# Performance work log

Hardware: AMD Instinct MI355X
Metric: run time of the kernel (lower is better)

The kernel has to match this reference:

```python
import jax, jax.numpy as jnp
import numpy as np

N, TP, E = 8, 2048, 4096
S = 8            # 2**spatial_dim
C = 64           # sqrt(embed_dim)
T = TP * S       # 16384
V = 16           # num_vocab


def setup_inputs() -> dict:
    key = jax.random.key(0)
    ks = jax.random.split(key, 9)
    x = jax.random.normal(ks[0], (N, TP, E), dtype=jnp.float32)
    value = jax.random.randint(ks[1], (N, T), 0, 4, dtype=jnp.int64)
    depth = jnp.sort(jax.random.randint(ks[2], (N, T), 0, 16, dtype=jnp.int64), axis=1)
    pos = jax.random.randint(ks[3], (N, T, 3), 0, 32, dtype=jnp.int64)
    # ConvTranspose1d(E, C, kernel=S, stride=S): weight [E, C, S]
    W1 = jax.random.normal(ks[4], (E, C, S), dtype=jnp.float32) / np.sqrt(E)
    b1 = jax.random.normal(ks[5], (C,), dtype=jnp.float32) * 0.01
    # ConvTranspose1d(C, 1, kernel=S, stride=S): weight [C, 1, S]
    W2 = jax.random.normal(ks[6], (C, 1, S), dtype=jnp.float32) / np.sqrt(C)
    b2 = jax.random.normal(ks[7], (1,), dtype=jnp.float32) * 0.01
    # Linear(1, V+1, bias=False): weight [V+1, 1]
    W3 = jax.random.normal(ks[8], (V + 1, 1), dtype=jnp.float32)
    return {"x": x, "value": value, "depth": depth, "pos": pos,
            "W1": W1, "b1": b1, "W2": W2, "b2": b2, "W3": W3}


def reference(x, value, depth, pos, W1, b1, W2, b2, W3):
    n, tp, e = x.shape
    s = W1.shape[2]
    t = value.shape[1]  # = tp * s
    posn = jnp.arange(t)
    # Truncate each value sequence at argmax(depth); pad_sequence pads with 0.
    idx = jnp.argmax(depth, axis=1)                      # [N]
    val_pad = jnp.where(posn[None, :] < idx[:, None], value, 0)  # [N, T]
    # deconv_1: stride == kernel -> non-overlapping expansion
    x1 = jnp.einsum('nte,ecs->ntsc', x, W1).reshape(n, t, -1) + b1  # [N, T, C]
    # Per-sample masked gather (val==2), compacted to front, zero-padded
    mask = val_pad == 2                                   # [N, T]
    order = jnp.argsort(jnp.logical_not(mask), axis=1, stable=True)  # True first
    y = jnp.take_along_axis(x1, order[:, :, None], axis=1)           # [N, T, C]
    counts = mask.sum(axis=1)                             # [N]
    y = jnp.where((posn[None, :] < counts[:, None])[:, :, None], y, 0.0)
    # deconv_2: [N, T, C] -> [N, T*S, 1]
    y2 = jnp.einsum('ntc,cs->nts', y, W2[:, 0, :]).reshape(n, t * s, 1) + b2
    # linear (no bias): [N, T*S, V+1]
    return y2 @ W3.T
```

## Files before the change

### kernel.cpp

```cpp
#include <hip/hip_runtime.h>

#define N_    8
#define TP_   2048
#define E_    4096
#define S_    8
#define C_    64
#define T_    16384
#define TS_   131072
#define OUTW  17
#define OUT_ELEMS 17825792
#define F4_PER_N 557056
#define F4_TOTAL 4456448

typedef __attribute__((ext_vector_type(8))) short short8;
typedef __attribute__((ext_vector_type(4))) float float4v;

static __device__ __forceinline__ unsigned short f2bf(float f) {
    unsigned int u = __builtin_bit_cast(unsigned int, f);
    u += 0x7FFFu + ((u >> 16) & 1u);
    return (unsigned short)(u >> 16);
}

__global__ __launch_bounds__(256) void prep_kernel(
    const float* __restrict__ W1, const float* __restrict__ b1,
    const float* __restrict__ W2, const float* __restrict__ b2,
    unsigned short* __restrict__ Bb, float* __restrict__ K2)
{
    __shared__ float tile[64][65];
    const int tid = threadIdx.x;
    if (blockIdx.x == 0 && blockIdx.y == 0 && tid < 8) {
        int s2 = tid;
        float acc = b2[0];
        for (int c = 0; c < C_; ++c) acc += b1[c] * W2[c * S_ + s2];
        K2[s2] = acc;
    }
    const int e0  = blockIdx.x * 64;
    const int cs0 = blockIdx.y * 64;
    {
        int rr = tid >> 2;
        int c4 = tid & 3;
        for (int i = 0; i < 4; ++i) {
            int f4 = c4 + i * 4;
            float4 v = *(const float4*)&W1[(size_t)(e0 + rr) * 512 + cs0 + f4 * 4];
            tile[f4 * 4 + 0][rr] = v.x;
            tile[f4 * 4 + 1][rr] = v.y;
            tile[f4 * 4 + 2][rr] = v.z;
            tile[f4 * 4 + 3][rr] = v.w;
        }
    }
    __syncthreads();
    {
        int cs  = tid >> 2;
        int seg = tid & 3;
        for (int h = 0; h < 2; ++h) {
            short8 o;
#pragma unroll
            for (int j = 0; j < 8; ++j)
                o[j] = (short)f2bf(tile[cs][seg * 16 + h * 8 + j]);
            *(short8*)&Bb[(size_t)(cs0 + cs) * E_ + e0 + seg * 16 + h * 8] = o;
        }
    }
}

__global__ __launch_bounds__(256) void compact_kernel(
    const int* __restrict__ value, const int* __restrict__ depth,
    int* __restrict__ cnt_ns, int* __restrict__ cnt_total,
    int* __restrict__ tile_counter, int* __restrict__ tiles,
    int* __restrict__ sel_tp, int* __restrict__ sel_j)
{
    const int g = blockIdx.x;
    const int n = g >> 3;
    const int s = g & 7;
    const int tid  = threadIdx.x;
    const int lane = tid & 63;
    const int wv   = tid >> 6;

    __shared__ int idx_sh;
    __shared__ unsigned int wsum[4];

    const int* d = depth + (size_t)n * T_;
    if (tid < 64) {
        int maxv = d[T_ - 1];
        int lower = 0, upper = T_ - 1;
        for (int rnd = 0; rnd < 3; ++rnd) {
            int span = upper - lower;
            int step = (span + 63) >> 6;
            if (step < 1) step = 1;
            int p = lower + lane * step;
            if (p > upper) p = upper;
            unsigned long long b = __ballot(d[p] == maxv);
            int f = __ffsll((long long)b) - 1;
            int nu = lower + f * step; if (nu > upper) nu = upper;
            int nl = (f == 0) ? lower : lower + (f - 1) * step + 1;
            if (nl > nu) nl = nu;
            lower = nl; upper = nu;
        }
        if (lane == 0) idx_sh = lower;
    }
    __syncthreads();
    const int idx = idx_sh;
    const int4* val4 = (const int4*)(value + (size_t)n * T_);

    const int b4 = tid * 16;
    unsigned int packed = 0;
    for (int i = 0; i < 16; ++i) {
        int4 v = val4[b4 + i];
        int t = (b4 + i) * 4;
        if (t + 0 < idx && v.x == 2) { packed += 0x10000u; if (((t + 0) & 7) == s) packed += 1u; }
        if (t + 1 < idx && v.y == 2) { packed += 0x10000u; if (((t + 1) & 7) == s) packed += 1u; }
        if (t + 2 < idx && v.z == 2) { packed += 0x10000u; if (((t + 2) & 7) == s) packed += 1u; }
        if (t + 3 < idx && v.w == 2) { packed += 0x10000u; if (((t + 3) & 7) == s) packed += 1u; }
    }
    unsigned int inc = packed;
#pragma unroll
    for (int off = 1; off < 64; off <<= 1) {
        unsigned int u = __shfl_up((int)inc, off, 64);
        if (lane >= off) inc += u;
    }
    if (lane == 63) wsum[wv] = inc;
    __syncthreads();
    unsigned int woff = 0;
    for (int ww = 0; ww < wv; ++ww) woff += wsum[ww];
    unsigned int excl = woff + inc - packed;
    int any_rank = (int)(excl >> 16);
    int s_rank   = (int)(excl & 0xFFFFu);
    for (int i = 0; i < 16; ++i) {
        int4 v = val4[b4 + i];
        int vv[4] = { v.x, v.y, v.z, v.w };
        int t = (b4 + i) * 4;
#pragma unroll
        for (int e = 0; e < 4; ++e) {
            int tt = t + e;
            if (tt < idx && vv[e] == 2) {
                if ((tt & 7) == s) {
                    sel_tp[g * 2048 + s_rank] = tt >> 3;
                    sel_j [g * 2048 + s_rank] = any_rank;
                    ++s_rank;
                }
                ++any_rank;
            }
        }
    }
    if (tid == 255) {
        unsigned int tot = woff + inc;
        int cnt = (int)(tot & 0xFFFFu);
        cnt_ns[g] = cnt;
        if (s == 0) cnt_total[n] = (int)(tot >> 16);
        int ntl = (cnt + 63) >> 6;
        int base = atomicAdd(tile_counter, ntl);
        for (int i = 0; i < ntl; ++i) tiles[base + i] = (g << 8) | i;
    }
}

__global__ __launch_bounds__(256) void fill_kernel(
    float* __restrict__ out, const float* __restrict__ W3,
    const float* __restrict__ b2, const int* __restrict__ cnt_total)
{
    __shared__ float pat[136];
    const int tid = threadIdx.x;
    if (tid < 136) pat[tid] = b2[0] * W3[tid % OUTW];
    __syncthreads();
    int i4 = blockIdx.x * 256 + tid;
    int n   = i4 / F4_PER_N;
    int rem = i4 - n * F4_PER_N;
    int j   = rem / 34;
    if (j >= cnt_total[n]) {
        int o = (rem - j * 34) * 4;
        float4 v = { pat[o], pat[o + 1], pat[o + 2], pat[o + 3] };
        *(float4*)&out[(size_t)i4 * 4] = v;
    }
}

__global__ __launch_bounds__(256) void main_kernel(
    const float* __restrict__ x, const unsigned short* __restrict__ Bb,
    const int* __restrict__ tile_counter, const int* __restrict__ tiles,
    const int* __restrict__ cnt_ns, const int* __restrict__ sel_tp,
    const int* __restrict__ sel_j, const float* __restrict__ K2,
    const float* __restrict__ W2, const float* __restrict__ W3,
    float* __restrict__ out)
{
    __shared__ __align__(16) char arena[36864];
    unsigned short (*bufA)[64][72] = (unsigned short (*)[64][72])arena;
    unsigned short (*bufB)[64][72] = (unsigned short (*)[64][72])(arena + 18432);
    float (*Cl)[68] = (float (*)[68])arena;
    float (*y2s)[8] = (float (*)[8])(arena + 17408);
    __shared__ int tp_l[64], j_l[64];
    __shared__ float W2s[C_ * S_];
    __shared__ float W3s[OUTW];
    __shared__ float K2s[S_];

    const int tid = threadIdx.x;
    for (int i = tid; i < C_ * S_; i += 256) W2s[i] = W2[i];
    if (tid < OUTW) W3s[tid] = W3[tid];
    if (tid < S_)   K2s[tid] = K2[tid];

    const int ntile = *tile_counter;

    const int lane = tid & 63;
    const int w    = tid >> 6;
    const int m    = lane & 15;
    const int q    = lane >> 4;
    const int r    = tid >> 4;
    const int kq   = (tid & 15) << 2;

    for (int ti = blockIdx.x; ti < ntile; ti += gridDim.x) {
        const int ent = tiles[ti];
        const int g = ent >> 8;
        const int n = g >> 3;
        const int s = g & 7;
        const int m0 = (ent & 255) * 64;
        const int rows = min(64, cnt_ns[g] - m0);

        __syncthreads();
        if (tid < 64) {
            int tp = 0, j = 0;
            if (tid < rows) {
                tp = sel_tp[g * 2048 + m0 + tid];
                j  = sel_j [g * 2048 + m0 + tid];
            }
            tp_l[tid] = tp;
            j_l[tid]  = j;
        }
        __syncthreads();

        const float* ap[4];
        const unsigned short* bp[4];
#pragma unroll
        for (int l = 0; l < 4; ++l) {
            int row = r + (l << 4);
            ap[l] = x + ((size_t)n * TP_ + tp_l[row]) * E_ + kq;
            bp[l] = Bb + ((size_t)(row * 8 + s)) * E_ + kq;
        }

        float4  Af0[4], Af1[4];
        ushort4 Bf0[4], Bf1[4];
#pragma unroll
        for (int l = 0; l < 4; ++l) {
            Af0[l] = *(const float4*)(ap[l]);
            Bf0[l] = *(const ushort4*)(bp[l]);
            Af1[l] = *(const float4*)(ap[l] + 64);
            Bf1[l] = *(const ushort4*)(bp[l] + 64);
        }

        float4v acc[4];
#pragma unroll
        for (int nt = 0; nt < 4; ++nt) acc[nt] = (float4v){0.f, 0.f, 0.f, 0.f};

#define GEMM_PHASE(P, AF, BF)                                                 \
        {                                                                     \
            _Pragma("unroll")                                                 \
            for (int l = 0; l < 4; ++l) {                                     \
                int row = r + (l << 4);                                       \
                ushort4 av;                                                   \
                av.x = f2bf(AF[l].x); av.y = f2bf(AF[l].y);                   \
                av.z = f2bf(AF[l].z); av.w = f2bf(AF[l].w);                   \
                *(ushort4*)&bufA[P][row][kq] = av;                            \
                *(ushort4*)&bufB[P][row][kq] = BF[l];                         \
            }                                                                 \
            __syncthreads();                                                  \
            if (kb + 2 + P < 64) {                                            \
                const int k0 = (kb + 2 + P) * 64;                             \
                _Pragma("unroll")                                             \
                for (int l = 0; l < 4; ++l) {                                 \
                    AF[l] = *(const float4*)(ap[l] + k0);                     \
                    BF[l] = *(const ushort4*)(bp[l] + k0);                    \
                }                                                             \
            }                                                                 \
            _Pragma("unroll")                                                 \
            for (int ks = 0; ks < 2; ++ks) {                                  \
                short8 a = *(const short8*)&bufA[P][w * 16 + m][ks * 32 + q * 8]; \
                _Pragma("unroll")                                             \
                for (int nt = 0; nt < 4; ++nt) {                              \
                    short8 b = *(const short8*)&bufB[P][nt * 16 + m][ks * 32 + q * 8]; \
                    acc[nt] = __builtin_amdgcn_mfma_f32_16x16x32_bf16(a, b, acc[nt], 0, 0, 0); \
                }                                                             \
            }                                                                 \
        }

        for (int kb = 0; kb < 64; kb += 2) {
            GEMM_PHASE(0, Af0, Bf0)
            GEMM_PHASE(1, Af1, Bf1)
        }
#undef GEMM_PHASE

        __syncthreads();

#pragma unroll
        for (int nt = 0; nt < 4; ++nt)
#pragma unroll
            for (int rr = 0; rr < 4; ++rr)
                Cl[w * 16 + q * 4 + rr][nt * 16 + m] = acc[nt][rr];
        __syncthreads();

        for (int task = tid; task < 512; task += 256) {
            int row = task >> 3;
            int s2  = task & 7;
            float y2 = K2s[s2];
#pragma unroll
            for (int c = 0; c < C_; ++c) y2 += Cl[row][c] * W2s[c * S_ + s2];
            y2s[row][s2] = y2;
        }
        __syncthreads();

        for (int task = tid; task < 64 * 34; task += 256) {
            int row = task / 34;
            int f   = task - row * 34;
            if (row < rows) {
                float4 v;
                float* vp = (float*)&v;
#pragma unroll
                for (int e = 0; e < 4; ++e) {
                    int idx = f * 4 + e;
                    int s2  = (idx * 241) >> 12;
                    int vi  = idx - s2 * OUTW;
                    vp[e] = y2s[row][s2] * W3s[vi];
                }
                *(float4*)&out[((size_t)n * TS_ + (size_t)j_l[row] * S_) * OUTW + f * 4] = v;
            }
        }
    }
}

extern "C" void kernel_launch(void* const* d_in, const int* in_sizes, int n_in,
                              void* d_out, int out_size, void* d_ws, size_t ws_size,
                              hipStream_t stream) {
    const float* x     = (const float*)d_in[0];
    const int*   value = (const int*)d_in[1];
    const int*   depth = (const int*)d_in[2];
    const float* W1    = (const float*)d_in[4];
    const float* b1    = (const float*)d_in[5];
    const float* W2    = (const float*)d_in[6];
    const float* b2    = (const float*)d_in[7];
    const float* W3    = (const float*)d_in[8];
    float* out = (float*)d_out;

    unsigned short* Bb = (unsigned short*)d_ws;
    float* K2          = (float*)(Bb + 512 * 4096);
    int* tile_counter  = (int*)(K2 + 8);
    int* cnt_ns        = tile_counter + 1;
    int* cnt_total     = cnt_ns + 64;
    int* tiles         = cnt_total + 8;
    int* sel_tp        = tiles + 2048;
    int* sel_j         = sel_tp + 64 * 2048;

    hipMemsetAsync(tile_counter, 0, sizeof(int), stream);

    dim3 pgrid(64, 8);
    prep_kernel<<<pgrid, 256, 0, stream>>>(W1, b1, W2, b2, Bb, K2);
    compact_kernel<<<64, 256, 0, stream>>>(value, depth, cnt_ns, cnt_total,
                                           tile_counter, tiles, sel_tp, sel_j);
    fill_kernel<<<F4_TOTAL / 256, 256, 0, stream>>>(out, W3, b2, cnt_total);
    main_kernel<<<512, 256, 0, stream>>>(x, Bb, tile_counter, tiles, cnt_ns,
                                         sel_tp, sel_j, K2, W2, W3, out);
}
```

Measured before the change: 443.9 us.

## Fold W2 into W1 to shrink GEMM width and fuse prep/compact/fill kernels

```diff
diff --git a/kernel.cpp b/kernel.cpp
--- a/kernel.cpp
+++ b/kernel.cpp
@@ -11,6 +11,10 @@
 #define OUT_ELEMS 17825792
 #define F4_PER_N 557056
 #define F4_TOTAL 4456448
+#define KSTEPS 128
+#define GEMM_BLOCKS 512
+#define FILL_BLOCKS 4352
+#define MPREP_BLOCKS 256
 
 typedef __attribute__((ext_vector_type(8))) short short8;
 typedef __attribute__((ext_vector_type(4))) float float4v;
@@ -20,190 +24,202 @@
     u += 0x7FFFu + ((u >> 16) & 1u);
     return (unsigned short)(u >> 16);
 }
-
-__global__ __launch_bounds__(256) void prep_kernel(
+static __device__ __forceinline__ float bf2f(unsigned short h) {
+    return __builtin_bit_cast(float, (unsigned int)h << 16);
+}
+
+__global__ __launch_bounds__(256) void prep_compact_kernel(
     const float* __restrict__ W1, const float* __restrict__ b1,
     const float* __restrict__ W2, const float* __restrict__ b2,
-    unsigned short* __restrict__ Bb, float* __restrict__ K2)
+    const int* __restrict__ value, const int* __restrict__ depth,
+    unsigned short* __restrict__ Mhi, unsigned short* __restrict__ Mlo,
+    float* __restrict__ K2,
+    int* __restrict__ cnt_ns, int* __restrict__ cnt_total,
+    int* __restrict__ tile_counter, int* __restrict__ tiles,
+    int* __restrict__ sel_tp, int* __restrict__ sel_j)
 {
-    __shared__ float tile[64][65];
     const int tid = threadIdx.x;
-    if (blockIdx.x == 0 && blockIdx.y == 0 && tid < 8) {
+    const int b   = blockIdx.x;
+
+    if (b < 64) {
+        __shared__ int idx_sh;
+        __shared__ unsigned int wsum[4];
+        const int g = b;
+        const int n = g >> 3;
+        const int s = g & 7;
+        const int lane = tid & 63;
+        const int wv   = tid >> 6;
+
+        const int* d = depth + (size_t)n * T_;
+        if (tid < 64) {
+            int maxv = d[T_ - 1];
+            int lower = 0, upper = T_ - 1;
+            for (int rnd = 0; rnd < 3; ++rnd) {
+                int span = upper - lower;
+                int step = (span + 63) >> 6;
+                if (step < 1) step = 1;
+                int p = lower + lane * step;
+                if (p > upper) p = upper;
+                unsigned long long bb = __ballot(d[p] == maxv);
+                int f = __ffsll((long long)bb) - 1;
+                int nu = lower + f * step; if (nu > upper) nu = upper;
+                int nl = (f == 0) ? lower : lower + (f - 1) * step + 1;
+                if (nl > nu) nl = nu;
+                lower = nl; upper = nu;
+            }
+            if (lane == 0) idx_sh = lower;
+        }
+        __syncthreads();
+        const int idx = idx_sh;
+        const int4* val4 = (const int4*)(value + (size_t)n * T_);
+
+        const int b4 = tid * 16;
+        unsigned int packed = 0;
+        for (int i = 0; i < 16; ++i) {
+            int4 v = val4[b4 + i];
+            int t = (b4 + i) * 4;
+            if (t + 0 < idx && v.x == 2) { packed += 0x10000u; if (((t + 0) & 7) == s) packed += 1u; }
+            if (t + 1 < idx && v.y == 2) { packed += 0x10000u; if (((t + 1) & 7) == s) packed += 1u; }
+            if (t + 2 < idx && v.z == 2) { packed += 0x10000u; if (((t + 2) & 7) == s) packed += 1u; }
+            if (t + 3 < idx && v.w == 2) { packed += 0x10000u; if (((t + 3) & 7) == s) packed += 1u; }
+        }
+        unsigned int inc = packed;
+#pragma unroll
+        for (int off = 1; off < 64; off <<= 1) {
+            unsigned int u = __shfl_up((int)inc, off, 64);
+            if (lane >= off) inc += u;
+        }
+        if (lane == 63) wsum[wv] = inc;
+        __syncthreads();
+        unsigned int woff = 0;
+        for (int ww = 0; ww < wv; ++ww) woff += wsum[ww];
+        unsigned int excl = woff + inc - packed;
+        int any_rank = (int)(excl >> 16);
+        int s_rank   = (int)(excl & 0xFFFFu);
+        for (int i = 0; i < 16; ++i) {
+            int4 v = val4[b4 + i];
+            int vv[4] = { v.x, v.y, v.z, v.w };
+            int t = (b4 + i) * 4;
+#pragma unroll
+            for (int e = 0; e < 4; ++e) {
+                int tt = t + e;
+                if (tt < idx && vv[e] == 2) {
+                    if ((tt & 7) == s) {
+                        sel_tp[g * 2048 + s_rank] = tt >> 3;
+                        sel_j [g * 2048 + s_rank] = any_rank;
+                        ++s_rank;
+                    }
+                    ++any_rank;
+                }
+            }
+        }
+        if (tid == 255) {
+            unsigned int tot = woff + inc;
+            int cnt = (int)(tot & 0xFFFFu);
+            cnt_ns[g] = cnt;
+            if (s == 0) cnt_total[n] = (int)(tot >> 16);
+            int ntl = (cnt + 63) >> 6;
+            int base = atomicAdd(tile_counter, ntl);
+            for (int i = 0; i < ntl; ++i) tiles[base + i] = (g << 8) | i;
+        }
+        return;
+    }
+
+    __shared__ float W1t[16 * 512];
+    __shared__ float W2s[512];
+
+    if (b == 64 && tid < 8) {
         int s2 = tid;
         float acc = b2[0];
         for (int c = 0; c < C_; ++c) acc += b1[c] * W2[c * S_ + s2];
         K2[s2] = acc;
     }
-    const int e0  = blockIdx.x * 64;
-    const int cs0 = blockIdx.y * 64;
+
+    const int kk    = b - 64;
+    const int kstep = kk >> 1;
+    const int h     = kk & 1;
+    const int k0    = kstep * 32 + h * 16;
+
+    for (int i = tid; i < 512; i += 256) W2s[i] = W2[i];
     {
-        int rr = tid >> 2;
-        int c4 = tid & 3;
-        for (int i = 0; i < 4; ++i) {
-            int f4 = c4 + i * 4;
-            float4 v = *(const float4*)&W1[(size_t)(e0 + rr) * 512 + cs0 + f4 * 4];
-            tile[f4 * 4 + 0][rr] = v.x;
-            tile[f4 * 4 + 1][rr] = v.y;
-            tile[f4 * 4 + 2][rr] = v.z;
-            tile[f4 * 4 + 3][rr] = v.w;
-        }
+        const float4* src = (const float4*)(W1 + (size_t)k0 * 512);
+        float4* dst = (float4*)W1t;
+        for (int i = tid; i < 16 * 128; i += 256) dst[i] = src[i];
     }
     __syncthreads();
-    {
-        int cs  = tid >> 2;
-        int seg = tid & 3;
-        for (int h = 0; h < 2; ++h) {
-            short8 o;
+
+    const int s    = tid >> 5;
+    const int lsub = tid & 31;
+    const int lane = h * 32 + lsub;
+    const int qq   = lsub >> 4;
+    const int s2   = lane & 15;
+
+    float accj[8] = {0.f,0.f,0.f,0.f,0.f,0.f,0.f,0.f};
+    if (s2 < 8) {
+        for (int c = 0; c < C_; ++c) {
+            float w2 = W2s[c * 8 + s2];
+            int base = c * 8 + s;
 #pragma unroll
             for (int j = 0; j < 8; ++j)
-                o[j] = (short)f2bf(tile[cs][seg * 16 + h * 8 + j]);
-            *(short8*)&Bb[(size_t)(cs0 + cs) * E_ + e0 + seg * 16 + h * 8] = o;
-        }
-    }
-}
-
-__global__ __launch_bounds__(256) void compact_kernel(
-    const int* __restrict__ value, const int* __restrict__ depth,
-    int* __restrict__ cnt_ns, int* __restrict__ cnt_total,
-    int* __restrict__ tile_counter, int* __restrict__ tiles,
-    int* __restrict__ sel_tp, int* __restrict__ sel_j)
-{
-    const int g = blockIdx.x;
-    const int n = g >> 3;
-    const int s = g & 7;
-    const int tid  = threadIdx.x;
-    const int lane = tid & 63;
-    const int wv   = tid >> 6;
-
-    __shared__ int idx_sh;
-    __shared__ unsigned int wsum[4];
-
-    const int* d = depth + (size_t)n * T_;
-    if (tid < 64) {
-        int maxv = d[T_ - 1];
-        int lower = 0, upper = T_ - 1;
-        for (int rnd = 0; rnd < 3; ++rnd) {
-            int span = upper - lower;
-            int step = (span + 63) >> 6;
-            if (step < 1) step = 1;
-            int p = lower + lane * step;
-            if (p > upper) p = upper;
-            unsigned long long b = __ballot(d[p] == maxv);
-            int f = __ffsll((long long)b) - 1;
-            int nu = lower + f * step; if (nu > upper) nu = upper;
-            int nl = (f == 0) ? lower : lower + (f - 1) * step + 1;
-            if (nl > nu) nl = nu;
-            lower = nl; upper = nu;
-        }
-        if (lane == 0) idx_sh = lower;
-    }
-    __syncthreads();
-    const int idx = idx_sh;
-    const int4* val4 = (const int4*)(value + (size_t)n * T_);
-
-    const int b4 = tid * 16;
-    unsigned int packed = 0;
-    for (int i = 0; i < 16; ++i) {
-        int4 v = val4[b4 + i];
-        int t = (b4 + i) * 4;
-        if (t + 0 < idx && v.x == 2) { packed += 0x10000u; if (((t + 0) & 7) == s) packed += 1u; }
-        if (t + 1 < idx && v.y == 2) { packed += 0x10000u; if (((t + 1) & 7) == s) packed += 1u; }
-        if (t + 2 < idx && v.z == 2) { packed += 0x10000u; if (((t + 2) & 7) == s) packed += 1u; }
-        if (t + 3 < idx && v.w == 2) { packed += 0x10000u; if (((t + 3) & 7) == s) packed += 1u; }
-    }
-    unsigned int inc = packed;
-#pragma unroll
-    for (int off = 1; off < 64; off <<= 1) {
-        unsigned int u = __shfl_up((int)inc, off, 64);
-        if (lane >= off) inc += u;
-    }
-    if (lane == 63) wsum[wv] = inc;
-    __syncthreads();
-    unsigned int woff = 0;
-    for (int ww = 0; ww < wv; ++ww) woff += wsum[ww];
-    unsigned int excl = woff + inc - packed;
-    int any_rank = (int)(excl >> 16);
-    int s_rank   = (int)(excl & 0xFFFFu);
-    for (int i = 0; i < 16; ++i) {
-        int4 v = val4[b4 + i];
-        int vv[4] = { v.x, v.y, v.z, v.w };
-        int t = (b4 + i) * 4;
-#pragma unroll
-        for (int e = 0; e < 4; ++e) {
-            int tt = t + e;
-            if (tt < idx && vv[e] == 2) {
-                if ((tt & 7) == s) {
-                    sel_tp[g * 2048 + s_rank] = tt >> 3;
-                    sel_j [g * 2048 + s_rank] = any_rank;
-                    ++s_rank;
-                }
-                ++any_rank;
-            }
-        }
-    }
-    if (tid == 255) {
-        unsigned int tot = woff + inc;
-        int cnt = (int)(tot & 0xFFFFu);
-        cnt_ns[g] = cnt;
-        if (s == 0) cnt_total[n] = (int)(tot >> 16);
-        int ntl = (cnt + 63) >> 6;
-        int base = atomicAdd(tile_counter, ntl);
-        for (int i = 0; i < ntl; ++i) tiles[base + i] = (g << 8) | i;
-    }
-}
-
-__global__ __launch_bounds__(256) void fill_kernel(
-    float* __restrict__ out, const float* __restrict__ W3,
-    const float* __restrict__ b2, const int* __restrict__ cnt_total)
-{
-    __shared__ float pat[136];
-    const int tid = threadIdx.x;
-    if (tid < 136) pat[tid] = b2[0] * W3[tid % OUTW];
-    __syncthreads();
-    int i4 = blockIdx.x * 256 + tid;
-    int n   = i4 / F4_PER_N;
-    int rem = i4 - n * F4_PER_N;
-    int j   = rem / 34;
-    if (j >= cnt_total[n]) {
-        int o = (rem - j * 34) * 4;
-        float4 v = { pat[o], pat[o + 1], pat[o + 2], pat[o + 3] };
-        *(float4*)&out[(size_t)i4 * 4] = v;
+                accj[j] += W1t[(qq * 8 + j) * 512 + base] * w2;
+        }
+    }
+    size_t o = ((size_t)(s * KSTEPS + kstep) * 64 + lane) * 8;
+#pragma unroll
+    for (int j = 0; j < 8; ++j) {
+        unsigned short hi = f2bf(accj[j]);
+        unsigned short lo = f2bf(accj[j] - bf2f(hi));
+        Mhi[o + j] = hi;
+        Mlo[o + j] = lo;
     }
 }
 
 __global__ __launch_bounds__(256) void main_kernel(
-    const float* __restrict__ x, const unsigned short* __restrict__ Bb,
+    const float* __restrict__ x,
+    const unsigned short* __restrict__ Mhi, const unsigned short* __restrict__ Mlo,
     const int* __restrict__ tile_counter, const int* __restrict__ tiles,
     const int* __restrict__ cnt_ns, const int* __restrict__ sel_tp,
     const int* __restrict__ sel_j, const float* __restrict__ K2,
-    const float* __restrict__ W2, const float* __restrict__ W3,
-    float* __restrict__ out)
+    const float* __restrict__ W3, const float* __restrict__ b2,
+    const int* __restrict__ cnt_total, float* __restrict__ out)
 {
-    __shared__ __align__(16) char arena[36864];
-    unsigned short (*bufA)[64][72] = (unsigned short (*)[64][72])arena;
-    unsigned short (*bufB)[64][72] = (unsigned short (*)[64][72])(arena + 18432);
-    float (*Cl)[68] = (float (*)[68])arena;
-    float (*y2s)[8] = (float (*)[8])(arena + 17408);
+    const int tid = threadIdx.x;
+
+    if (blockIdx.x >= GEMM_BLOCKS) {
+        __shared__ float pat[136];
+        if (tid < 136) pat[tid] = b2[0] * W3[tid % OUTW];
+        __syncthreads();
+        const int fb = blockIdx.x - GEMM_BLOCKS;
+#pragma unroll
+        for (int it = 0; it < 4; ++it) {
+            int i4 = fb * 1024 + it * 256 + tid;
+            int n   = i4 / F4_PER_N;
+            int rem = i4 - n * F4_PER_N;
+            int j   = rem / 34;
+            if (j >= cnt_total[n]) {
+                int o = (rem - j * 34) * 4;
+                float4 v = { pat[o], pat[o + 1], pat[o + 2], pat[o + 3] };
+                *(float4*)&out[(size_t)i4 * 4] = v;
+            }
+        }
+        return;
+    }
+
     __shared__ int tp_l[64], j_l[64];
-    __shared__ float W2s[C_ * S_];
+    __shared__ float y2s[64][8];
     __shared__ float W3s[OUTW];
     __shared__ float K2s[S_];
 
-    const int tid = threadIdx.x;
-    for (int i = tid; i < C_ * S_; i += 256) W2s[i] = W2[i];
     if (tid < OUTW) W3s[tid] = W3[tid];
     if (tid < S_)   K2s[tid] = K2[tid];
 
     const int ntile = *tile_counter;
-
     const int lane = tid & 63;
     const int w    = tid >> 6;
     const int m    = lane & 15;
     const int q    = lane >> 4;
-    const int r    = tid >> 4;
-    const int kq   = (tid & 15) << 2;
-
-    for (int ti = blockIdx.x; ti < ntile; ti += gridDim.x) {
+
+    for (int ti = blockIdx.x; ti < ntile; ti += GEMM_BLOCKS) {
         const int ent = tiles[ti];
         const int g = ent >> 8;
         const int n = g >> 3;
@@ -223,82 +239,50 @@
         }
         __syncthreads();
 
-        const float* ap[4];
-        const unsigned short* bp[4];
-#pragma unroll
-        for (int l = 0; l < 4; ++l) {
-            int row = r + (l << 4);
-            ap[l] = x + ((size_t)n * TP_ + tp_l[row]) * E_ + kq;
-            bp[l] = Bb + ((size_t)(row * 8 + s)) * E_ + kq;
-        }
-
-        float4  Af0[4], Af1[4];
-        ushort4 Bf0[4], Bf1[4];
-#pragma unroll
-        for (int l = 0; l < 4; ++l) {
-            Af0[l] = *(const float4*)(ap[l]);
-            Bf0[l] = *(const ushort4*)(bp[l]);
-            Af1[l] = *(const float4*)(ap[l] + 64);
-            Bf1[l] = *(const ushort4*)(bp[l] + 64);
-        }
-
-        float4v acc[4];
-#pragma unroll
-        for (int nt = 0; nt < 4; ++nt) acc[nt] = (float4v){0.f, 0.f, 0.f, 0.f};
-
-#define GEMM_PHASE(P, AF, BF)                                                 \
-        {                                                                     \
-            _Pragma("unroll")                                                 \
-            for (int l = 0; l < 4; ++l) {                                     \
-                int row = r + (l << 4);                                       \
-                ushort4 av;                                                   \
-                av.x = f2bf(AF[l].x); av.y = f2bf(AF[l].y);                   \
-                av.z = f2bf(AF[l].z); av.w = f2bf(AF[l].w);                   \
-                *(ushort4*)&bufA[P][row][kq] = av;                            \
-                *(ushort4*)&bufB[P][row][kq] = BF[l];                         \
-            }                                                                 \
-            __syncthreads();                                                  \
-            if (kb + 2 + P < 64) {                                            \
-                const int k0 = (kb + 2 + P) * 64;                             \
-                _Pragma("unroll")                                             \
-                for (int l = 0; l < 4; ++l) {                                 \
-                    AF[l] = *(const float4*)(ap[l] + k0);                     \
-                    BF[l] = *(const ushort4*)(bp[l] + k0);                    \
-                }                                                             \
-            }                                                                 \
-            _Pragma("unroll")                                                 \
-            for (int ks = 0; ks < 2; ++ks) {                                  \
-                short8 a = *(const short8*)&bufA[P][w * 16 + m][ks * 32 + q * 8]; \
-                _Pragma("unroll")                                             \
-                for (int nt = 0; nt < 4; ++nt) {                              \
-                    short8 b = *(const short8*)&bufB[P][nt * 16 + m][ks * 32 + q * 8]; \
-                    acc[nt] = __builtin_amdgcn_mfma_f32_16x16x32_bf16(a, b, acc[nt], 0, 0, 0); \
-                }                                                             \
-            }                                                                 \
-        }
-
-        for (int kb = 0; kb < 64; kb += 2) {
-            GEMM_PHASE(0, Af0, Bf0)
-            GEMM_PHASE(1, Af1, Bf1)
-        }
-#undef GEMM_PHASE
-
-        __syncthreads();
-
-#pragma unroll
-        for (int nt = 0; nt < 4; ++nt)
+        const float* arow = x + ((size_t)n * TP_ + tp_l[w * 16 + m]) * E_ + q * 8;
+        const unsigned short* bh = Mhi + ((size_t)s * KSTEPS * 64 + lane) * 8;
+        const unsigned short* bl = Mlo + ((size_t)s * KSTEPS * 64 + lane) * 8;
+
+        float4v acc = {0.f, 0.f, 0.f, 0.f};
+
+        float4 A00 = *(const float4*)(arow);
+        float4 A01 = *(const float4*)(arow + 4);
+        short8 Bh0 = *(const short8*)(bh);
+        short8 Bl0 = *(const short8*)(bl);
+        float4 A10 = *(const float4*)(arow + 32);
+        float4 A11 = *(const float4*)(arow + 36);
+        short8 Bh1 = *(const short8*)(bh + 512);
+        short8 Bl1 = *(const short8*)(bl + 512);
+
+#define STEP(P, A0, A1, BH, BL)                                                \
+        {                                                                      \
+            short8 av;                                                         \
+            av[0] = (short)f2bf(A0.x); av[1] = (short)f2bf(A0.y);              \
+            av[2] = (short)f2bf(A0.z); av[3] = (short)f2bf(A0.w);              \
+            av[4] = (short)f2bf(A1.x); av[5] = (short)f2bf(A1.y);              \
+            av[6] = (short)f2bf(A1.z); av[7] = (short)f2bf(A1.w);              \
+            short8 bhc = BH, blc = BL;                                         \
+            if (ks + 2 + P < KSTEPS) {                                         \
+                const float* ap = arow + (size_t)(ks + 2 + P) * 32;            \
+                A0 = *(const float4*)(ap);                                     \
+                A1 = *(const float4*)(ap + 4);                                 \
+                BH = *(const short8*)(bh + (size_t)(ks + 2 + P) * 512);        \
+                BL = *(const short8*)(bl + (size_t)(ks + 2 + P) * 512);        \
+            }                                                                  \
+            acc = __builtin_amdgcn_mfma_f32_16x16x32_bf16(av, bhc, acc, 0, 0, 0); \
+            acc = __builtin_amdgcn_mfma_f32_16x16x32_bf16(av, blc, acc, 0, 0, 0); \
+        }
+
+        for (int ks = 0; ks < KSTEPS; ks += 2) {
+            STEP(0, A00, A01, Bh0, Bl0)
+            STEP(1, A10, A11, Bh1, Bl1)
+        }
+#undef STEP
+
+        if (m < 8) {
 #pragma unroll
             for (int rr = 0; rr < 4; ++rr)
-                Cl[w * 16 + q * 4 + rr][nt * 16 + m] = acc[nt][rr];
-        __syncthreads();
-
-        for (int task = tid; task < 512; task += 256) {
-            int row = task >> 3;
-            int s2  = task & 7;
-            float y2 = K2s[s2];
-#pragma unroll
-            for (int c = 0; c < C_; ++c) y2 += Cl[row][c] * W2s[c * S_ + s2];
-            y2s[row][s2] = y2;
+                y2s[w * 16 + q * 4 + rr][m] = acc[rr] + K2s[m];
         }
         __syncthreads();
 
@@ -334,8 +318,9 @@
     const float* W3    = (const float*)d_in[8];
     float* out = (float*)d_out;
 
-    unsigned short* Bb = (unsigned short*)d_ws;
-    float* K2          = (float*)(Bb + 512 * 4096);
+    unsigned short* Mhi = (unsigned short*)d_ws;
+    unsigned short* Mlo = Mhi + 8 * KSTEPS * 64 * 8;
+    float* K2          = (float*)(Mlo + 8 * KSTEPS * 64 * 8);
     int* tile_counter  = (int*)(K2 + 8);
     int* cnt_ns        = tile_counter + 1;
     int* cnt_total     = cnt_ns + 64;
@@ -345,11 +330,11 @@
 
     hipMemsetAsync(tile_counter, 0, sizeof(int), stream);
 
-    dim3 pgrid(64, 8);
-    prep_kernel<<<pgrid, 256, 0, stream>>>(W1, b1, W2, b2, Bb, K2);
-    compact_kernel<<<64, 256, 0, stream>>>(value, depth, cnt_ns, cnt_total,
-                                           tile_counter, tiles, sel_tp, sel_j);
-    fill_kernel<<<F4_TOTAL / 256, 256, 0, stream>>>(out, W3, b2, cnt_total);
-    main_kernel<<<512, 256, 0, stream>>>(x, Bb, tile_counter, tiles, cnt_ns,
-                                         sel_tp, sel_j, K2, W2, W3, out);
-}
+    prep_compact_kernel<<<64 + MPREP_BLOCKS, 256, 0, stream>>>(
+        W1, b1, W2, b2, value, depth, Mhi, Mlo, K2,
+        cnt_ns, cnt_total, tile_counter, tiles, sel_tp, sel_j);
+
+    main_kernel<<<GEMM_BLOCKS + FILL_BLOCKS, 256, 0, stream>>>(
+        x, Mhi, Mlo, tile_counter, tiles, cnt_ns, sel_tp, sel_j,
+        K2, W3, b2, cnt_total, out);
+}
```

Result: slower. 456.1 us (+2.8%).
